# Kernel optimization log

Hardware: AMD Instinct MI355X
Metric: run time of the kernel (lower is better)

The kernel has to match this reference:

```python
import jax, jax.numpy as jnp
import numpy as np

D1 = 3          # elevated lattice dim (self.d == self.d1 == 3 in source)
S = 384         # size2d = 128*3
B, N = 32, 65536

# canonical simplex offsets, built exactly as in __init__
_c = np.tile(np.arange(D1), (D1, 1))
for _i in range(1, D1):
    _c[-_i:, _i] = _i - D1
CANONICAL = jnp.asarray(_c, dtype=jnp.int32)  # [[0,1,2],[0,1,-1],[0,-2,-1]]


def setup_inputs() -> dict:
    key = jax.random.key(0)
    k1, k2, k3 = jax.random.split(key, 3)
    # get_model.scalePoints rescales coords to ~0.8*size2d; emulate that range
    pc1 = jax.random.uniform(k1, (B, 3, N), dtype=jnp.float32) * (0.8 * S)
    features = jax.random.normal(k2, (B, 3, N), dtype=jnp.float32)
    tm = jax.random.normal(k3, (B, 3, 3), dtype=jnp.float32)
    # F.normalize(trans_matrix, dim=1)
    trans_mat = tm / jnp.maximum(jnp.linalg.norm(tm, axis=1, keepdims=True), 1e-12)
    return {"pc1": pc1, "features": features, "trans_mat": trans_mat}


def _keys_and_barycentric(pc, trans_mat):
    b, _, n = pc.shape
    elevated = jnp.einsum('bij,bjn->bin', trans_mat, pc)          # (B,3,N)
    greedy = jnp.round(elevated / D1) * D1
    emg = elevated - greedy
    # rank = inverse permutation of descending argsort over the 3 lattice dims
    order = jnp.argsort(-emg, axis=1)
    rank = jnp.argsort(order, axis=1).astype(jnp.int32)           # (B,3,N)
    rs = jnp.sum(greedy, axis=1, keepdims=True) / D1              # (B,1,N)
    rf = rank.astype(jnp.float32)
    cond = (((rf >= D1 - rs) & (rs > 0)) | ((rf < -rs) & (rs < 0))).astype(jnp.float32)
    sign = jnp.where(rs > 0, -1.0, 0.0) + jnp.where(rs < 0, 1.0, 0.0)
    greedy = greedy + D1 * sign * cond
    rank = rank + (D1 * sign * cond).astype(jnp.int32)
    rank = rank + rs.astype(jnp.int32)
    emg2 = elevated - greedy
    greedy_i = greedy.astype(jnp.int32)
    b_ix = jnp.arange(b)[:, None, None]
    n_ix = jnp.arange(n)[None, None, :]
    # NOTE: source uses self.d - rank for += and self.d1 - rank for -=, but d==d1,
    # so the two scatter-adds cancel exactly; barycentric degenerates to [1,0,0].
    # Reproduce the same computation faithfully.
    bary = jnp.zeros((b, D1 + 1, n), jnp.float32)
    bary = bary.at[b_ix, D1 - rank, n_ix].add(emg2)
    bary = bary.at[b_ix, D1 - rank, n_ix].add(-emg2)
    bary = bary / D1
    bary = bary.at[:, 0, :].add(1.0 + bary[:, D1, :])
    bary = bary[:, :D1, :]                                        # (B,3,N)
    keys = greedy_i[:, :, :, None] + CANONICAL[rank]              # (B,3,N,3)
    return keys, bary


def reference(pc1, features, trans_mat):
    keys, bary = _keys_and_barycentric(pc1, trans_mat)
    b = features.shape[0]
    coord = keys[:, :2].reshape(b, 2, -1)                          # (B,2,3N)
    offset = coord.min(axis=2)                                     # (B,2) int
    coord = coord - offset[:, :, None]
    # tmp[b, n*3+j, c] = bary[b, j, n] * features[b, c, n]
    tmp = bary[:, None, :, :] * features[:, :, None, :]            # (B,3,3,N)
    tmp = jnp.transpose(tmp, (0, 1, 3, 2)).reshape(b, 3, -1)       # (B,3,3N)
    tmp = jnp.transpose(tmp, (0, 2, 1))                            # (B,3N,3)
    pts_pick = (-offset) % D1                                      # (B,2)
    oob = coord >= S
    coord = jnp.where(oob, 0, coord)
    bad = jnp.sum(oob, axis=1) > 0                                 # (B,3N)
    tmp = jnp.where(bad[:, :, None], 0.0, tmp)

    ar = jnp.arange(S // D1)

    def splat_one(cd, vals, pick):
        sp = jnp.zeros((S, S, 3), jnp.float32).at[cd[0], cd[1]].add(vals)
        return sp[pick[0] + D1 * ar][:, pick[1] + D1 * ar]

    filter_2d = jax.vmap(splat_one)(coord, tmp, pts_pick)          # (B,S/3,S/3,3)
    return filter_2d
```

## Files before the change

### kernel.cpp

```cpp
#include <hip/hip_runtime.h>
#include <stdint.h>

#define NPTS 65536
#define NB   32
#define SS   384

#define C3INV 0.333333343267440796f

#define FP_SCALE 32768.0f
#define FP_INV   (1.0f / 32768.0f)

__device__ __forceinline__ float fmul_strict(float a, float b) {
    float r;
    asm volatile("v_mul_f32 %0, %1, %2" : "=v"(r) : "v"(a), "v"(b));
    return r;
}
__device__ __forceinline__ float fadd_strict(float a, float b) {
    float r;
    asm volatile("v_add_f32 %0, %1, %2" : "=v"(r) : "v"(a), "v"(b));
    return r;
}

__device__ __forceinline__ void lattice_point(
    const float* __restrict__ t,
    float p0, float p1, float p2,
    int& gi0, int& gi1, int& rc0, int& rc1)
{
    float e0 = fadd_strict(fadd_strict(fmul_strict(t[0], p0), fmul_strict(t[1], p1)), fmul_strict(t[2], p2));
    float e1 = fadd_strict(fadd_strict(fmul_strict(t[3], p0), fmul_strict(t[4], p1)), fmul_strict(t[5], p2));
    float e2 = fadd_strict(fadd_strict(fmul_strict(t[6], p0), fmul_strict(t[7], p1)), fmul_strict(t[8], p2));

    float g0 = __fmul_rn(rintf(__fmul_rn(e0, C3INV)), 3.0f);
    float g1 = __fmul_rn(rintf(__fmul_rn(e1, C3INV)), 3.0f);
    float g2 = __fmul_rn(rintf(__fmul_rn(e2, C3INV)), 3.0f);

    float m0 = e0 - g0, m1 = e1 - g1, m2 = e2 - g2;
    int r0 = (int)(m1 > m0) + (int)(m2 > m0);
    int r1 = (int)(m0 >= m1) + (int)(m2 > m1);

    gi0 = (int)g0;
    gi1 = (int)g1;

    const int irs = (gi0 + gi1 + (int)g2) / 3;

    if (irs > 0) {
        if (r0 >= 3 - irs) { gi0 -= 3; r0 -= 3; }
        if (r1 >= 3 - irs) { gi1 -= 3; r1 -= 3; }
    } else if (irs < 0) {
        if (r0 < -irs) { gi0 += 3; r0 += 3; }
        if (r1 < -irs) { gi1 += 3; r1 += 3; }
    }
    r0 += irs;
    r1 += irs;

    if (r0 < 0) r0 += 3;
    if (r1 < 0) r1 += 3;
    rc0 = min(2, max(0, r0));
    rc1 = min(2, max(0, r1));
}

__device__ __forceinline__ int icl3(int a) {
    return (a >= 0) ? (a + 2) / 3 : -((-a) / 3);
}

__global__ __launch_bounds__(1024) void bin_kernel(
    const float* __restrict__ pc, const float* __restrict__ tmg,
    uint32_t* __restrict__ bins, int* __restrict__ partial)
{
    const int bx  = blockIdx.x;
    const int b   = blockIdx.y;
    const int tid = threadIdx.x;

    __shared__ float t[9];
    if (tid < 9) t[tid] = tmg[b * 9 + tid];
    __syncthreads();

    const float* pcb = pc + (size_t)b * 3 * NPTS;
    const int v = bx * 1024 + tid;

    const float4 P0 = ((const float4*)(pcb + 0 * NPTS))[v];
    const float4 P1 = ((const float4*)(pcb + 1 * NPTS))[v];
    const float4 P2 = ((const float4*)(pcb + 2 * NPTS))[v];

    int km0 = 0x7FFFFFFF, km1 = 0x7FFFFFFF;
    uint32_t pk[4];
    const float p0a[4] = {P0.x, P0.y, P0.z, P0.w};
    const float p1a[4] = {P1.x, P1.y, P1.z, P1.w};
    const float p2a[4] = {P2.x, P2.y, P2.z, P2.w};
#pragma unroll
    for (int i = 0; i < 4; ++i) {
        int gi0, gi1, rc0, rc1;
        lattice_point(t, p0a[i], p1a[i], p2a[i], gi0, gi1, rc0, rc1);
        pk[i] = (uint32_t)(((gi0 / 3 + 512) << 16) | (gi1 / 3 + 512));
        km0 = min(km0, gi0 - rc0);
        km1 = min(km1, gi1 - rc1);
    }
    ((uint4*)(bins + (size_t)b * NPTS))[v] = make_uint4(pk[0], pk[1], pk[2], pk[3]);

#pragma unroll
    for (int off = 32; off > 0; off >>= 1) {
        km0 = min(km0, __shfl_down(km0, off));
        km1 = min(km1, __shfl_down(km1, off));
    }
    __shared__ int s0[16], s1[16];
    if ((tid & 63) == 0) { s0[tid >> 6] = km0; s1[tid >> 6] = km1; }
    __syncthreads();
    if (tid == 0) {
        int m0 = s0[0], m1 = s1[0];
#pragma unroll
        for (int j = 1; j < 16; ++j) { m0 = min(m0, s0[j]); m1 = min(m1, s1[j]); }
        partial[(b * 16 + bx) * 2 + 0] = m0;
        partial[(b * 16 + bx) * 2 + 1] = m1;
    }
}

#define CH_HIST 16384

__global__ __launch_bounds__(1024) void splat_ch_stage_kernel(
    const uint32_t* __restrict__ bins, const float* __restrict__ feat,
    const int* __restrict__ partial, int* __restrict__ stg)
{
    const int b     = blockIdx.x;
    const int ch    = blockIdx.y;
    const int chunk = blockIdx.z;
    const int tid   = threadIdx.x;

    __shared__ __align__(16) int ihist[CH_HIST];
#pragma unroll
    for (int j = 0; j < 4; ++j)
        ((int4*)ihist)[j * 1024 + tid] = make_int4(0, 0, 0, 0);

    int off0 = 0x7FFFFFFF, off1 = 0x7FFFFFFF;
#pragma unroll
    for (int j = 0; j < 16; ++j) {
        off0 = min(off0, partial[(b * 16 + j) * 2 + 0]);
        off1 = min(off1, partial[(b * 16 + j) * 2 + 1]);
    }
    __syncthreads();

    const int K0 = 512 + icl3(off0);
    const int K1 = 512 + icl3(off1);

    const uint32_t* bb = bins + (size_t)b * NPTS + (size_t)chunk * (NPTS / 4);
    const float*    fb = feat + ((size_t)b * 3 + ch) * NPTS + (size_t)chunk * (NPTS / 4);

#pragma unroll
    for (int i = 0; i < (NPTS / 4) / 4096; ++i) {
        const int v = i * 1024 + tid;
        const uint4  U = ((const uint4 *)bb)[v];
        const float4 F = ((const float4*)fb)[v];

        const uint32_t ua[4] = {U.x, U.y, U.z, U.w};
        const float    fa[4] = {F.x, F.y, F.z, F.w};

#pragma unroll
        for (int k = 0; k < 4; ++k) {
            const int y = (int)(ua[k] >> 16) - K0;
            const int x = (int)(ua[k] & 0xFFFFu) - K1;
            if (y < 128 && x < 128) {
                const int q = (int)rintf(__fmul_rn(fa[k], FP_SCALE));
                atomicAdd(&ihist[(y << 7) + x], q);
            }
        }
    }
    __syncthreads();

    int4* dst = (int4*)(stg + (size_t)(((b * 3 + ch) << 2) + chunk) * CH_HIST);
#pragma unroll
    for (int j = 0; j < 4; ++j)
        dst[j * 1024 + tid] = ((const int4*)ihist)[j * 1024 + tid];
}

__global__ __launch_bounds__(1024) void sum_convert_kernel(
    const int* __restrict__ stg, float* __restrict__ out)
{
    const int t = blockIdx.x * 1024 + threadIdx.x;
    const int b = blockIdx.y;

    float o[12];
#pragma unroll
    for (int ch = 0; ch < 3; ++ch) {
        const int4* s = (const int4*)(stg + (size_t)((b * 3 + ch) << 2) * CH_HIST);
        const int4 a0 = s[t];
        const int4 a1 = s[t + 1 * (CH_HIST / 4)];
        const int4 a2 = s[t + 2 * (CH_HIST / 4)];
        const int4 a3 = s[t + 3 * (CH_HIST / 4)];
        const int vx = a0.x + a1.x + a2.x + a3.x;
        const int vy = a0.y + a1.y + a2.y + a3.y;
        const int vz = a0.z + a1.z + a2.z + a3.z;
        const int vw = a0.w + a1.w + a2.w + a3.w;
        o[0 * 3 + ch] = __fmul_rn((float)vx, FP_INV);
        o[1 * 3 + ch] = __fmul_rn((float)vy, FP_INV);
        o[2 * 3 + ch] = __fmul_rn((float)vz, FP_INV);
        o[3 * 3 + ch] = __fmul_rn((float)vw, FP_INV);
    }

    float4* op = (float4*)(out + ((size_t)((b << 14) + t * 4)) * 3);
    op[0] = make_float4(o[0], o[1],  o[2],  o[3]);
    op[1] = make_float4(o[4], o[5],  o[6],  o[7]);
    op[2] = make_float4(o[8], o[9],  o[10], o[11]);
}

__global__ __launch_bounds__(1024) void splat_ch_int_kernel(
    const uint32_t* __restrict__ bins, const float* __restrict__ feat,
    const int* __restrict__ partial, int* __restrict__ iout)
{
    const int b     = blockIdx.x;
    const int ch    = blockIdx.y;
    const int chunk = blockIdx.z;
    const int tid   = threadIdx.x;

    __shared__ int ihist[CH_HIST];
#pragma unroll
    for (int i = tid; i < CH_HIST; i += 1024) ihist[i] = 0;

    int off0 = 0x7FFFFFFF, off1 = 0x7FFFFFFF;
#pragma unroll
    for (int j = 0; j < 16; ++j) {
        off0 = min(off0, partial[(b * 16 + j) * 2 + 0]);
        off1 = min(off1, partial[(b * 16 + j) * 2 + 1]);
    }
    __syncthreads();

    const int K0 = 512 + icl3(off0);
    const int K1 = 512 + icl3(off1);

    const uint32_t* bb = bins + (size_t)b * NPTS + (size_t)chunk * (NPTS / 4);
    const float*    fb = feat + ((size_t)b * 3 + ch) * NPTS + (size_t)chunk * (NPTS / 4);

#pragma unroll
    for (int i = 0; i < (NPTS / 4) / 4096; ++i) {
        const int v = i * 1024 + tid;
        const uint4  U = ((const uint4 *)bb)[v];
        const float4 F = ((const float4*)fb)[v];
        const uint32_t ua[4] = {U.x, U.y, U.z, U.w};
        const float    fa[4] = {F.x, F.y, F.z, F.w};
#pragma unroll
        for (int k = 0; k < 4; ++k) {
            const int y = (int)(ua[k] >> 16) - K0;
            const int x = (int)(ua[k] & 0xFFFFu) - K1;
            if (y < 128 && x < 128) {
                const int q = (int)rintf(__fmul_rn(fa[k], FP_SCALE));
                atomicAdd(&ihist[(y << 7) + x], q);
            }
        }
    }
    __syncthreads();

#pragma unroll
    for (int i = tid; i < CH_HIST; i += 1024) {
        const int v = ihist[i];
        if (v != 0) atomicAdd(&iout[(size_t)((b << 14) + i) * 3 + ch], v);
    }
}

__global__ __launch_bounds__(1024) void convert_kernel(float* __restrict__ out)
{
    const int i = blockIdx.x * 1024 + threadIdx.x;
    const int v = ((const int*)out)[i];
    out[i] = __fmul_rn((float)v, FP_INV);
}

#define FTILE_X 16
#define FHIST_F (128 * FTILE_X * 3)

__global__ __launch_bounds__(1024) void kmin2_kernel(
    const float* __restrict__ pc, const float* __restrict__ tmg,
    int* __restrict__ mins)
{
    const int b = blockIdx.y, bx = blockIdx.x, tid = threadIdx.x;
    __shared__ float t[9];
    if (tid < 9) t[tid] = tmg[b * 9 + tid];
    __syncthreads();

    const float* pcb = pc + (size_t)b * 3 * NPTS;
    int km0 = 0x7FFFFFFF, km1 = 0x7FFFFFFF;
    const int n0 = bx * 8192;
#pragma unroll
    for (int i = 0; i < 8; ++i) {
        const int n = n0 + i * 1024 + tid;
        int gi0, gi1, rc0, rc1;
        lattice_point(t, pcb[n], pcb[NPTS + n], pcb[2 * NPTS + n], gi0, gi1, rc0, rc1);
        km0 = min(km0, gi0 - rc0);
        km1 = min(km1, gi1 - rc1);
    }
#pragma unroll
    for (int off = 32; off > 0; off >>= 1) {
        km0 = min(km0, __shfl_down(km0, off));
        km1 = min(km1, __shfl_down(km1, off));
    }
    __shared__ int s0[16], s1[16];
    if ((tid & 63) == 0) { s0[tid >> 6] = km0; s1[tid >> 6] = km1; }
    __syncthreads();
    if (tid == 0) {
        int m0 = s0[0], m1 = s1[0];
#pragma unroll
        for (int j = 1; j < 16; ++j) { m0 = min(m0, s0[j]); m1 = min(m1, s1[j]); }
        atomicMin(&mins[b * 2 + 0], m0);
        atomicMin(&mins[b * 2 + 1], m1);
    }
}

__global__ __launch_bounds__(1024) void splat_recompute_kernel(
    const float* __restrict__ pc, const float* __restrict__ feat,
    const float* __restrict__ tmg, const int* __restrict__ mins,
    float* __restrict__ out)
{
    const int tile = blockIdx.x, b = blockIdx.y, tid = threadIdx.x;
    const int x0 = tile * FTILE_X;

    __shared__ float t[9];
    __shared__ float hist[FHIST_F];
    if (tid < 9) t[tid] = tmg[b * 9 + tid];
#pragma unroll
    for (int i = tid; i < FHIST_F; i += 1024) hist[i] = 0.0f;
    __syncthreads();

    const int off0 = mins[b * 2 + 0];
    const int off1 = mins[b * 2 + 1];
    const float* pcb = pc + (size_t)b * 3 * NPTS;
    const float* ftb = feat + (size_t)b * 3 * NPTS;

    for (int n = tid; n < NPTS; n += 1024) {
        int gi0, gi1, rc0, rc1;
        lattice_point(t, pcb[n], pcb[NPTS + n], pcb[2 * NPTS + n], gi0, gi1, rc0, rc1);
        const int c0 = gi0 - off0;
        const int c1 = gi1 - off1;
        if ((unsigned)c0 < SS && (unsigned)c1 < SS) {
            const int x = c1 / 3;
            if ((x >> 4) == tile) {
                const int y = c0 / 3;
                const int base = (y * FTILE_X + (x - x0)) * 3;
                atomicAdd(&hist[base + 0], ftb[0 * NPTS + n]);
                atomicAdd(&hist[base + 1], ftb[1 * NPTS + n]);
                atomicAdd(&hist[base + 2], ftb[2 * NPTS + n]);
            }
        }
    }
    __syncthreads();
#pragma unroll
    for (int idx = tid; idx < FHIST_F; idx += 1024) {
        const int y   = idx / (FTILE_X * 3);
        const int rem = idx - y * (FTILE_X * 3);
        out[(size_t)(b * 128 + y) * 384 + x0 * 3 + rem] = hist[idx];
    }
}

extern "C" void kernel_launch(void* const* d_in, const int* in_sizes, int n_in,
                              void* d_out, int out_size, void* d_ws, size_t ws_size,
                              hipStream_t stream) {
    const float* pc   = (const float*)d_in[0];
    const float* feat = (const float*)d_in[1];
    const float* tm   = (const float*)d_in[2];
    float* out = (float*)d_out;

    const size_t bins_bytes = (size_t)NB * NPTS * sizeof(uint32_t);
    const size_t part_bytes = 1024 * sizeof(int);
    const size_t stg_bytes  = (size_t)NB * 3 * 4 * CH_HIST * sizeof(int);

    if (ws_size >= bins_bytes + part_bytes + stg_bytes) {
        uint32_t* bins = (uint32_t*)d_ws;
        int* partial = (int*)((char*)d_ws + bins_bytes);
        int* stg     = (int*)((char*)d_ws + bins_bytes + part_bytes);

        dim3 gridA(16, NB);
        bin_kernel<<<gridA, 1024, 0, stream>>>(pc, tm, bins, partial);
        dim3 gridB(NB, 3, 4);
        splat_ch_stage_kernel<<<gridB, 1024, 0, stream>>>(bins, feat, partial, stg);
        dim3 gridC(4, NB);
        sum_convert_kernel<<<gridC, 1024, 0, stream>>>(stg, out);
    } else if (ws_size >= bins_bytes + part_bytes) {
        uint32_t* bins = (uint32_t*)d_ws;
        int* partial = (int*)((char*)d_ws + bins_bytes);

        hipMemsetAsync(out, 0, (size_t)out_size * sizeof(float), stream);

        dim3 gridA(16, NB);
        bin_kernel<<<gridA, 1024, 0, stream>>>(pc, tm, bins, partial);
        dim3 gridB(NB, 3, 4);
        splat_ch_int_kernel<<<gridB, 1024, 0, stream>>>(bins, feat, partial, (int*)out);
        convert_kernel<<<(out_size + 1023) / 1024, 1024, 0, stream>>>(out);
    } else {
        int* mins = (int*)d_ws;
        hipMemsetAsync(mins, 0x7F, 64 * sizeof(int), stream);
        dim3 grid(8, NB);
        kmin2_kernel<<<grid, 1024, 0, stream>>>(pc, tm, mins);
        dim3 gridB2(8, NB);
        splat_recompute_kernel<<<gridB2, 1024, 0, stream>>>(pc, feat, tm, mins, out);
    }
}
```

Before: 102.0 us.

## Fuse binning, splatting and reduction into one cooperative kernel with grid syncs

```diff
diff --git a/kernel.cpp b/kernel.cpp
--- a/kernel.cpp
+++ b/kernel.cpp
@@ -1,5 +1,8 @@
 #include <hip/hip_runtime.h>
+#include <hip/hip_cooperative_groups.h>
 #include <stdint.h>
+
+namespace cg = cooperative_groups;
 
 #define NPTS 65536
 #define NB   32
@@ -63,6 +66,157 @@
     return (a >= 0) ? (a + 2) / 3 : -((-a) / 3);
 }
 
+#define CH_HIST 16384
+
+#define FBLOCKS  384
+#define FTHREADS 512
+#define FSLICES  12
+#define GRP_PER_B     (NPTS / 4)
+#define GRP_PER_SLICE 1366
+
+__global__ __launch_bounds__(FTHREADS, 4) void fused_kernel(
+    const float* __restrict__ pc, const float* __restrict__ feat,
+    const float* __restrict__ tmg, uint32_t* __restrict__ bins,
+    int* __restrict__ partial, int* __restrict__ stg, float* __restrict__ out)
+{
+    const int bid = blockIdx.x;
+    const int tid = threadIdx.x;
+    const int b   = bid & 31;
+    const int s   = bid >> 5;
+
+    __shared__ __align__(16) int ihist[CH_HIST];
+    float* t_sh = (float*)ihist;
+    int*   r0   = ihist + 12;
+    int*   r1   = ihist + 24;
+
+    cg::grid_group grid = cg::this_grid();
+
+    if (tid < 9) t_sh[tid] = tmg[b * 9 + tid];
+    __syncthreads();
+
+    const float* pcb = pc + (size_t)b * 3 * NPTS;
+    int km0 = 0x7FFFFFFF, km1 = 0x7FFFFFFF;
+    const int gbeg = s * GRP_PER_SLICE;
+    const int gend = min(GRP_PER_B, gbeg + GRP_PER_SLICE);
+
+    for (int v = gbeg + tid; v < gend; v += FTHREADS) {
+        const float4 P0 = ((const float4*)(pcb + 0 * NPTS))[v];
+        const float4 P1 = ((const float4*)(pcb + 1 * NPTS))[v];
+        const float4 P2 = ((const float4*)(pcb + 2 * NPTS))[v];
+
+        uint32_t pk[4];
+        const float p0a[4] = {P0.x, P0.y, P0.z, P0.w};
+        const float p1a[4] = {P1.x, P1.y, P1.z, P1.w};
+        const float p2a[4] = {P2.x, P2.y, P2.z, P2.w};
+#pragma unroll
+        for (int i = 0; i < 4; ++i) {
+            int gi0, gi1, rc0, rc1;
+            lattice_point(t_sh, p0a[i], p1a[i], p2a[i], gi0, gi1, rc0, rc1);
+            pk[i] = (uint32_t)(((gi0 / 3 + 512) << 16) | (gi1 / 3 + 512));
+            km0 = min(km0, gi0 - rc0);
+            km1 = min(km1, gi1 - rc1);
+        }
+        ((uint4*)(bins + (size_t)b * NPTS))[v] = make_uint4(pk[0], pk[1], pk[2], pk[3]);
+    }
+
+#pragma unroll
+    for (int off = 32; off > 0; off >>= 1) {
+        km0 = min(km0, __shfl_down(km0, off));
+        km1 = min(km1, __shfl_down(km1, off));
+    }
+    if ((tid & 63) == 0) { r0[tid >> 6] = km0; r1[tid >> 6] = km1; }
+    __syncthreads();
+    if (tid == 0) {
+        int m0 = r0[0], m1 = r1[0];
+#pragma unroll
+        for (int j = 1; j < FTHREADS / 64; ++j) { m0 = min(m0, r0[j]); m1 = min(m1, r1[j]); }
+        partial[bid * 2 + 0] = m0;
+        partial[bid * 2 + 1] = m1;
+    }
+
+    __threadfence();
+    grid.sync();
+
+    const int ch    = s >> 2;
+    const int chunk = s & 3;
+
+#pragma unroll
+    for (int j = 0; j < CH_HIST / 4 / FTHREADS; ++j)
+        ((int4*)ihist)[j * FTHREADS + tid] = make_int4(0, 0, 0, 0);
+
+    int off0 = 0x7FFFFFFF, off1 = 0x7FFFFFFF;
+#pragma unroll
+    for (int j = 0; j < FSLICES; ++j) {
+        off0 = min(off0, partial[((j << 5) | b) * 2 + 0]);
+        off1 = min(off1, partial[((j << 5) | b) * 2 + 1]);
+    }
+    __syncthreads();
+
+    const int K0 = 512 + icl3(off0);
+    const int K1 = 512 + icl3(off1);
+
+    const uint32_t* bb = bins + (size_t)b * NPTS + (size_t)chunk * (NPTS / 4);
+    const float*    fb = feat + ((size_t)b * 3 + ch) * NPTS + (size_t)chunk * (NPTS / 4);
+
+#pragma unroll
+    for (int i = 0; i < (NPTS / 4) / (4 * FTHREADS); ++i) {
+        const int v = i * FTHREADS + tid;
+        const uint4  U = ((const uint4 *)bb)[v];
+        const float4 F = ((const float4*)fb)[v];
+
+        const uint32_t ua[4] = {U.x, U.y, U.z, U.w};
+        const float    fa[4] = {F.x, F.y, F.z, F.w};
+
+#pragma unroll
+        for (int k = 0; k < 4; ++k) {
+            const int y = (int)(ua[k] >> 16) - K0;
+            const int x = (int)(ua[k] & 0xFFFFu) - K1;
+            if (y < 128 && x < 128) {
+                const int q = (int)rintf(__fmul_rn(fa[k], FP_SCALE));
+                atomicAdd(&ihist[(y << 7) + x], q);
+            }
+        }
+    }
+    __syncthreads();
+
+    int4* dst = (int4*)(stg + (size_t)(((b * 3 + ch) << 2) + chunk) * CH_HIST);
+#pragma unroll
+    for (int j = 0; j < CH_HIST / 4 / FTHREADS; ++j)
+        dst[j * FTHREADS + tid] = ((const int4*)ihist)[j * FTHREADS + tid];
+
+    __threadfence();
+    grid.sync();
+
+    const int w = bid * FTHREADS + tid;
+    if (w < NB * 4096) {
+        const int b3 = w >> 12;
+        const int t3 = w & 4095;
+
+        float o[12];
+#pragma unroll
+        for (int c = 0; c < 3; ++c) {
+            const int4* sp = (const int4*)(stg + (size_t)((b3 * 3 + c) << 2) * CH_HIST);
+            const int4 a0 = sp[t3];
+            const int4 a1 = sp[t3 + 1 * (CH_HIST / 4)];
+            const int4 a2 = sp[t3 + 2 * (CH_HIST / 4)];
+            const int4 a3 = sp[t3 + 3 * (CH_HIST / 4)];
+            const int vx = a0.x + a1.x + a2.x + a3.x;
+            const int vy = a0.y + a1.y + a2.y + a3.y;
+            const int vz = a0.z + a1.z + a2.z + a3.z;
+            const int vw = a0.w + a1.w + a2.w + a3.w;
+            o[0 * 3 + c] = __fmul_rn((float)vx, FP_INV);
+            o[1 * 3 + c] = __fmul_rn((float)vy, FP_INV);
+            o[2 * 3 + c] = __fmul_rn((float)vz, FP_INV);
+            o[3 * 3 + c] = __fmul_rn((float)vw, FP_INV);
+        }
+
+        float4* op = (float4*)(out + ((size_t)((b3 << 14) + t3 * 4)) * 3);
+        op[0] = make_float4(o[0], o[1],  o[2],  o[3]);
+        op[1] = make_float4(o[4], o[5],  o[6],  o[7]);
+        op[2] = make_float4(o[8], o[9],  o[10], o[11]);
+    }
+}
+
 __global__ __launch_bounds__(1024) void bin_kernel(
     const float* __restrict__ pc, const float* __restrict__ tmg,
     uint32_t* __restrict__ bins, int* __restrict__ partial)
@@ -113,8 +267,6 @@
         partial[(b * 16 + bx) * 2 + 1] = m1;
     }
 }
-
-#define CH_HIST 16384
 
 __global__ __launch_bounds__(1024) void splat_ch_stage_kernel(
     const uint32_t* __restrict__ bins, const float* __restrict__ feat,
@@ -355,10 +507,39 @@
     float* out = (float*)d_out;
 
     const size_t bins_bytes = (size_t)NB * NPTS * sizeof(uint32_t);
-    const size_t part_bytes = 1024 * sizeof(int);
+    const size_t part_bytes = 4096;
     const size_t stg_bytes  = (size_t)NB * 3 * 4 * CH_HIST * sizeof(int);
-
-    if (ws_size >= bins_bytes + part_bytes + stg_bytes) {
+    const size_t need_full  = bins_bytes + part_bytes + stg_bytes;
+
+    static int coop_ok = -1;
+    if (coop_ok < 0) {
+        int dev = 0;
+        hipDeviceProp_t prop;
+        if (hipGetDevice(&dev) == hipSuccess &&
+            hipGetDeviceProperties(&prop, dev) == hipSuccess)
+            coop_ok = prop.cooperativeLaunch ? 1 : 0;
+        else
+            coop_ok = 0;
+    }
+
+    if (coop_ok == 1 && ws_size >= need_full) {
+        uint32_t* bins = (uint32_t*)d_ws;
+        int* partial = (int*)((char*)d_ws + bins_bytes);
+        int* stg     = (int*)((char*)d_ws + bins_bytes + part_bytes);
+
+        const float* a_pc = pc; const float* a_feat = feat; const float* a_tm = tm;
+        uint32_t* a_bins = bins; int* a_partial = partial; int* a_stg = stg;
+        float* a_out = out;
+        void* args[] = {&a_pc, &a_feat, &a_tm, &a_bins, &a_partial, &a_stg, &a_out};
+
+        hipError_t e = hipLaunchCooperativeKernel(
+            (const void*)fused_kernel, dim3(FBLOCKS), dim3(FTHREADS),
+            args, 0, stream);
+        if (e == hipSuccess) return;
+        coop_ok = 0;
+    }
+
+    if (ws_size >= need_full) {
         uint32_t* bins = (uint32_t*)d_ws;
         int* partial = (int*)((char*)d_ws + bins_bytes);
         int* stg     = (int*)((char*)d_ws + bins_bytes + part_bytes);
```

Result: slower. 352.5 us (+245.6%).

## Fuse partial-histogram reduction into splat kernel via last-block ticket

Applied to the files above, without the earlier changes.

```diff
diff --git a/kernel.cpp b/kernel.cpp
--- a/kernel.cpp
+++ b/kernel.cpp
@@ -63,13 +63,19 @@
     return (a >= 0) ? (a + 2) / 3 : -((-a) / 3);
 }
 
+#define CH_HIST 16384
+
+
 __global__ __launch_bounds__(1024) void bin_kernel(
     const float* __restrict__ pc, const float* __restrict__ tmg,
-    uint32_t* __restrict__ bins, int* __restrict__ partial)
+    uint32_t* __restrict__ bins, int* __restrict__ partial,
+    int* __restrict__ tickets)
 {
     const int bx  = blockIdx.x;
     const int b   = blockIdx.y;
     const int tid = threadIdx.x;
+
+    if (bx == 0 && tid < 3) tickets[b * 3 + tid] = 0;
 
     __shared__ float t[9];
     if (tid < 9) t[tid] = tmg[b * 9 + tid];
@@ -114,11 +120,10 @@
     }
 }
 
-#define CH_HIST 16384
-
-__global__ __launch_bounds__(1024) void splat_ch_stage_kernel(
+__global__ __launch_bounds__(1024) void splat_finalize_kernel(
     const uint32_t* __restrict__ bins, const float* __restrict__ feat,
-    const int* __restrict__ partial, int* __restrict__ stg)
+    const int* __restrict__ partial, int* __restrict__ tickets,
+    int* __restrict__ stg, float* __restrict__ out)
 {
     const int b     = blockIdx.x;
     const int ch    = blockIdx.y;
@@ -165,40 +170,48 @@
     }
     __syncthreads();
 
-    int4* dst = (int4*)(stg + (size_t)(((b * 3 + ch) << 2) + chunk) * CH_HIST);
+    int* slice_base = stg + ((size_t)(b * 3 + ch) * 4 + chunk) * CH_HIST;
+    int4* dst = (int4*)slice_base;
 #pragma unroll
     for (int j = 0; j < 4; ++j)
         dst[j * 1024 + tid] = ((const int4*)ihist)[j * 1024 + tid];
-}
-
-__global__ __launch_bounds__(1024) void sum_convert_kernel(
-    const int* __restrict__ stg, float* __restrict__ out)
-{
-    const int t = blockIdx.x * 1024 + threadIdx.x;
-    const int b = blockIdx.y;
-
-    float o[12];
-#pragma unroll
-    for (int ch = 0; ch < 3; ++ch) {
-        const int4* s = (const int4*)(stg + (size_t)((b * 3 + ch) << 2) * CH_HIST);
-        const int4 a0 = s[t];
-        const int4 a1 = s[t + 1 * (CH_HIST / 4)];
-        const int4 a2 = s[t + 2 * (CH_HIST / 4)];
-        const int4 a3 = s[t + 3 * (CH_HIST / 4)];
+
+    __syncthreads();
+
+    __shared__ int lastFlag;
+    if (tid == 0) {
+        __threadfence();
+        const int old = atomicAdd(&tickets[b * 3 + ch], 1);
+        lastFlag = (old == 3);
+    }
+    __syncthreads();
+    if (!lastFlag) return;
+
+    __threadfence();
+
+    const int4* sl0 = (const int4*)(stg + ((size_t)(b * 3 + ch) * 4 + 0) * CH_HIST);
+    const int4* sl1 = (const int4*)(stg + ((size_t)(b * 3 + ch) * 4 + 1) * CH_HIST);
+    const int4* sl2 = (const int4*)(stg + ((size_t)(b * 3 + ch) * 4 + 2) * CH_HIST);
+    const int4* sl3 = (const int4*)(stg + ((size_t)(b * 3 + ch) * 4 + 3) * CH_HIST);
+
+#pragma unroll
+    for (int j = 0; j < 4; ++j) {
+        const int t = j * 1024 + tid;
+        const int4 a0 = sl0[t];
+        const int4 a1 = sl1[t];
+        const int4 a2 = sl2[t];
+        const int4 a3 = sl3[t];
         const int vx = a0.x + a1.x + a2.x + a3.x;
         const int vy = a0.y + a1.y + a2.y + a3.y;
         const int vz = a0.z + a1.z + a2.z + a3.z;
         const int vw = a0.w + a1.w + a2.w + a3.w;
-        o[0 * 3 + ch] = __fmul_rn((float)vx, FP_INV);
-        o[1 * 3 + ch] = __fmul_rn((float)vy, FP_INV);
-        o[2 * 3 + ch] = __fmul_rn((float)vz, FP_INV);
-        o[3 * 3 + ch] = __fmul_rn((float)vw, FP_INV);
-    }
-
-    float4* op = (float4*)(out + ((size_t)((b << 14) + t * 4)) * 3);
-    op[0] = make_float4(o[0], o[1],  o[2],  o[3]);
-    op[1] = make_float4(o[4], o[5],  o[6],  o[7]);
-    op[2] = make_float4(o[8], o[9],  o[10], o[11]);
+
+        float* op = out + ((size_t)((b << 14) + t * 4)) * 3 + ch;
+        op[0] = __fmul_rn((float)vx, FP_INV);
+        op[3] = __fmul_rn((float)vy, FP_INV);
+        op[6] = __fmul_rn((float)vz, FP_INV);
+        op[9] = __fmul_rn((float)vw, FP_INV);
+    }
 }
 
 __global__ __launch_bounds__(1024) void splat_ch_int_kernel(
@@ -355,28 +368,31 @@
     float* out = (float*)d_out;
 
     const size_t bins_bytes = (size_t)NB * NPTS * sizeof(uint32_t);
-    const size_t part_bytes = 1024 * sizeof(int);
+    const size_t part_bytes = 4096;
+    const size_t tick_bytes = 512;
     const size_t stg_bytes  = (size_t)NB * 3 * 4 * CH_HIST * sizeof(int);
-
-    if (ws_size >= bins_bytes + part_bytes + stg_bytes) {
+    const size_t need_full  = bins_bytes + part_bytes + tick_bytes + stg_bytes;
+
+    if (ws_size >= need_full) {
         uint32_t* bins = (uint32_t*)d_ws;
         int* partial = (int*)((char*)d_ws + bins_bytes);
-        int* stg     = (int*)((char*)d_ws + bins_bytes + part_bytes);
+        int* tickets = (int*)((char*)d_ws + bins_bytes + part_bytes);
+        int* stg     = (int*)((char*)d_ws + bins_bytes + part_bytes + tick_bytes);
 
         dim3 gridA(16, NB);
-        bin_kernel<<<gridA, 1024, 0, stream>>>(pc, tm, bins, partial);
+        bin_kernel<<<gridA, 1024, 0, stream>>>(pc, tm, bins, partial, tickets);
         dim3 gridB(NB, 3, 4);
-        splat_ch_stage_kernel<<<gridB, 1024, 0, stream>>>(bins, feat, partial, stg);
-        dim3 gridC(4, NB);
-        sum_convert_kernel<<<gridC, 1024, 0, stream>>>(stg, out);
-    } else if (ws_size >= bins_bytes + part_bytes) {
+        splat_finalize_kernel<<<gridB, 1024, 0, stream>>>(bins, feat, partial,
+                                                          tickets, stg, out);
+    } else if (ws_size >= bins_bytes + part_bytes + tick_bytes) {
         uint32_t* bins = (uint32_t*)d_ws;
         int* partial = (int*)((char*)d_ws + bins_bytes);
+        int* tickets = (int*)((char*)d_ws + bins_bytes + part_bytes);
 
         hipMemsetAsync(out, 0, (size_t)out_size * sizeof(float), stream);
 
         dim3 gridA(16, NB);
-        bin_kernel<<<gridA, 1024, 0, stream>>>(pc, tm, bins, partial);
+        bin_kernel<<<gridA, 1024, 0, stream>>>(pc, tm, bins, partial, tickets);
         dim3 gridB(NB, 3, 4);
         splat_ch_int_kernel<<<gridB, 1024, 0, stream>>>(bins, feat, partial, (int*)out);
         convert_kernel<<<(out_size + 1023) / 1024, 1024, 0, stream>>>(out);
```

New measurement: 178.4 us. +75.0%, slower.
